# Optimization experiments

Measured on AMD Instinct MI355X. Metric: run time of the kernel, lower is better.

The kernel has to match this reference:

```python
import jax, jax.numpy as jnp
import numpy as np

B, L, H = 8, 4096, 1024
S = 32            # sentences (sep tokens) per sample, fixed for stackability
SEP_ID = 102      # BERT [SEP]
NUM_LABELS = 2
LN_EPS = 1e-5


def _make_ids_and_mask():
    rng = np.random.default_rng(0)
    ids = rng.integers(1000, 30000, size=(B, L))
    for i in range(B):
        pos = np.sort(rng.choice(np.arange(1, L), size=S, replace=False))
        ids[i, pos] = SEP_ID
    mask = np.ones((B, L), dtype=np.int32)
    return jnp.asarray(ids, dtype=jnp.int64), jnp.asarray(mask)


def setup_inputs() -> dict:
    key = jax.random.key(0)
    ks = jax.random.split(key, 4)
    input_ids, attention_mask = _make_ids_and_mask()
    std = 0.02
    return {
        "seq": jax.random.normal(ks[0], (B, L, H), dtype=jnp.float32),
        "input_ids": input_ids,
        "attention_mask": attention_mask,
        "W1": jax.random.normal(ks[1], (H, H), dtype=jnp.float32) * std,
        "b1": jnp.zeros((H,), jnp.float32),
        "ln_g": jnp.ones((H,), jnp.float32),
        "ln_b": jnp.zeros((H,), jnp.float32),
        "W2": jax.random.normal(ks[2], (H, NUM_LABELS), dtype=jnp.float32) * std,
        "b2": jnp.zeros((NUM_LABELS,), jnp.float32),
    }


def _segment_means(seq, input_ids, attention_mask):
    # sep positions per sample, fixed count S -> [B, S]
    sep_pos = jax.vmap(
        lambda ids: jnp.nonzero(ids == SEP_ID, size=S, fill_value=L - 1)[0]
    )(input_ids)
    bounds = jnp.concatenate(
        [jnp.zeros((seq.shape[0], 1), sep_pos.dtype), sep_pos], axis=1
    )  # [B, S+1]
    st, ed = bounds[:, :-1], bounds[:, 1:]  # inclusive span [st, ed]

    m = attention_mask.astype(seq.dtype)[..., None]            # [B,L,1]
    # exclusive prefix sums -> sum over [st, ed] = P[ed+1] - P[st]
    P = jnp.pad(jnp.cumsum(seq * m, axis=1), ((0, 0), (1, 0), (0, 0)))   # [B,L+1,H]
    C = jnp.pad(jnp.cumsum(attention_mask.astype(jnp.int32), axis=1), ((0, 0), (1, 0)))

    sums = (jnp.take_along_axis(P, (ed + 1)[..., None], axis=1)
            - jnp.take_along_axis(P, st[..., None], axis=1))   # [B,S,H]
    cnts = (jnp.take_along_axis(C, ed + 1, axis=1)
            - jnp.take_along_axis(C, st, axis=1))              # [B,S]
    cnts = jnp.maximum(cnts, 1).astype(seq.dtype)
    return sums / cnts[..., None]


def reference(seq, input_ids, attention_mask, W1, b1, ln_g, ln_b, W2, b2):
    reps = _segment_means(seq, input_ids, attention_mask)      # [B,S,H]
    h = jnp.einsum("bsh,hk->bsk", reps, W1) + b1
    mu = jnp.mean(h, axis=-1, keepdims=True)
    var = jnp.var(h, axis=-1, keepdims=True)
    h = (h - mu) * jax.lax.rsqrt(var + LN_EPS) * ln_g + ln_b
    h = jax.nn.gelu(h, approximate=False)   # torch nn.GELU default (erf); dropout is eval-mode identity
    return jnp.einsum("bsk,kn->bsn", h, W2) + b2               # [B,S,num_labels]
```

## Files before the change

### kernel.cpp

```cpp
#include <hip/hip_runtime.h>
#include <math.h>

#define BB 8
#define LL 4096
#define HH 1024
#define SS 32
#define SEPID 102
#define NROWS 256
#define TOK 64
#define SPLITK 8
#define KSLICE (HH / SPLITK)

__global__ __launch_bounds__(256) void prep_kernel(
    const int* __restrict__ ids, const int* __restrict__ mask,
    float* __restrict__ cnts, int* __restrict__ spos_g,
    float* __restrict__ sums) {
  int b = blockIdx.x;
  int by = blockIdx.y;
  int tid = threadIdx.x;
  if (by > 0) {
    int z = b * 8 + (by - 1);
    float4 zero = make_float4(0.f, 0.f, 0.f, 0.f);
    float4* p = (float4*)sums + (size_t)z * 1024;
#pragma unroll
    for (int i = 0; i < 4; i++) p[tid + i * 256] = zero;
    return;
  }
  __shared__ int spos_raw[SS];
  __shared__ int spos[SS];
  __shared__ int nsep;
  __shared__ int excl_s[257];
  __shared__ int wtot[4];
  if (tid == 0) nsep = 0;
  if (tid < SS) spos_raw[tid] = LL - 1;
  __syncthreads();
  const int* idb = ids + (size_t)b * LL;
  const int* mb  = mask + (size_t)b * LL;

  for (int t = tid; t < LL; t += 256) {
    if (idb[t] == SEPID) {
      int slot = atomicAdd(&nsep, 1);
      if (slot < SS) spos_raw[slot] = t;
    }
  }
  __syncthreads();
  if (tid < SS) {
    int p = spos_raw[tid];
    int rank = 0;
    for (int j = 0; j < SS; j++) {
      int q = spos_raw[j];
      rank += (q < p) || (q == p && j < tid);
    }
    spos[rank] = p;
  }

  int local = 0;
  int base = tid * 16;
#pragma unroll
  for (int i = 0; i < 16; i++) local += mb[base + i];
  int lane = tid & 63, wave = tid >> 6;
  int v = local;
#pragma unroll
  for (int off = 1; off < 64; off <<= 1) {
    int n = __shfl_up(v, off, 64);
    if (lane >= off) v += n;
  }
  if (lane == 63) wtot[wave] = v;
  __syncthreads();
  int woff = 0;
  for (int w = 0; w < wave; w++) woff += wtot[w];
  excl_s[tid] = woff + v - local;
  if (tid == 0) excl_s[256] = wtot[0] + wtot[1] + wtot[2] + wtot[3];
  __syncthreads();

  if (tid < SS) {
    spos_g[b * SS + tid] = spos[tid];
    int st = (tid == 0) ? 0 : spos[tid - 1];
    int ed = spos[tid];
    int pa = st, pb = ed + 1;
    int ca = excl_s[pa >> 4];
    for (int i = pa & ~15; i < pa; i++) ca += mb[i];
    int cb = excl_s[pb >> 4];
    for (int i = pb & ~15; i < pb; i++) cb += mb[i];
    cnts[b * SS + tid] = (float)max(cb - ca, 1);
  }
}

__device__ __forceinline__ void flush_seg(float* __restrict__ sums, int b,
                                          int seg, int tid, const float4& acc) {
  if (seg >= 0) {
    float* p = sums + ((size_t)(b * SS + seg)) * HH + tid * 4;
    atomicAdd(p + 0, acc.x);
    atomicAdd(p + 1, acc.y);
    atomicAdd(p + 2, acc.z);
    atomicAdd(p + 3, acc.w);
  }
}

__global__ __launch_bounds__(256) void segsum_kernel(
    const float4* __restrict__ seq, const int* __restrict__ mask,
    const int* __restrict__ spos_g, float* __restrict__ sums) {
  const int chunks = LL / TOK;
  int b = blockIdx.x / chunks;
  int c = blockIdx.x % chunks;
  int t0 = c * TOK;
  int tid = threadIdx.x;
  __shared__ int sposs[SS];
  __shared__ int scode[TOK];
  if (tid < SS) sposs[tid] = spos_g[b * SS + tid];
  __syncthreads();
  if (t0 > sposs[SS - 1]) return;
  if (tid < TOK) {
    int t = t0 + tid;
    int lo = 0, hi = SS;
    while (lo < hi) {
      int mid = (lo + hi) >> 1;
      if (sposs[mid] < t) lo = mid + 1; else hi = mid;
    }
    int issep = (lo < SS && sposs[lo] == t) ? 1 : 0;
    int r = lo;
    int m = mask[(size_t)b * LL + t];
    int live = (issep || r < SS) ? 1 : 0;
    scode[tid] = ((r << 1) | issep) | ((m && live) ? 0x100 : 0);
  }
  __syncthreads();
  float4 acc = make_float4(0.f, 0.f, 0.f, 0.f);
  int curseg = -1;
  const int rs = HH / 4;
  const float4* rowbase = seq + (size_t)(b * LL + t0) * rs + tid;
  float4 cur[4], nxt[4];
#pragma unroll
  for (int j = 0; j < 4; j++) cur[j] = rowbase[(size_t)j * rs];
  for (int g = 0; g < TOK / 4; g++) {
    int tb = g * 4;
    if (g < TOK / 4 - 1) {
#pragma unroll
      for (int j = 0; j < 4; j++) nxt[j] = rowbase[(size_t)(tb + 4 + j) * rs];
    }
#pragma unroll
    for (int j = 0; j < 4; j++) {
      int cd = scode[tb + j];
      int r = (cd >> 1) & 0x3F;
      int issep = cd & 1;
      float mf = (cd & 0x100) ? 1.f : 0.f;
      float4 v = cur[j];
      v.x *= mf; v.y *= mf; v.z *= mf; v.w *= mf;
      if (issep) {
        if (curseg != r) {
          flush_seg(sums, b, curseg, tid, acc);
          acc = make_float4(0.f, 0.f, 0.f, 0.f);
        }
        acc.x += v.x; acc.y += v.y; acc.z += v.z; acc.w += v.w;
        flush_seg(sums, b, r, tid, acc);
        if (r + 1 < SS) { curseg = r + 1; acc = v; }
        else { curseg = -1; acc = make_float4(0.f, 0.f, 0.f, 0.f); }
      } else {
        int sg = (r < SS) ? r : -1;
        if (sg != curseg) {
          flush_seg(sums, b, curseg, tid, acc);
          curseg = sg;
          acc = make_float4(0.f, 0.f, 0.f, 0.f);
        }
        acc.x += v.x; acc.y += v.y; acc.z += v.z; acc.w += v.w;
      }
    }
#pragma unroll
    for (int j = 0; j < 4; j++) cur[j] = nxt[j];
  }
  flush_seg(sums, b, curseg, tid, acc);
}

__global__ __launch_bounds__(256) void gemm1_kernel(
    const float* __restrict__ sums, const float* __restrict__ W1,
    float* __restrict__ h1p) {
  __shared__ float As[32][68];
  __shared__ float Bs[32][68];
  int bj = blockIdx.x;
  int bi = blockIdx.y;
  int bz = blockIdx.z;
  int tid = threadIdx.x;
  int r0 = bi * 64, c0 = bj * 64, kb = bz * KSLICE;

  int ai = tid >> 3;
  int af = tid & 7;
  int bk = tid >> 4;
  int bj4 = tid & 15;
  int tx = tid & 15, ty = tid >> 4;

  float acc[4][4];
#pragma unroll
  for (int i = 0; i < 4; i++)
#pragma unroll
    for (int j = 0; j < 4; j++) acc[i][j] = 0.f;

  for (int k0 = kb; k0 < kb + KSLICE; k0 += 32) {
    if (k0 != kb) __syncthreads();
    float4 a0 = *(const float4*)&sums[(size_t)(r0 + ai) * HH + k0 + af * 4];
    float4 a1 = *(const float4*)&sums[(size_t)(r0 + ai + 32) * HH + k0 + af * 4];
    float4 b0 = *(const float4*)&W1[(size_t)(k0 + bk) * HH + c0 + bj4 * 4];
    float4 b1 = *(const float4*)&W1[(size_t)(k0 + bk + 16) * HH + c0 + bj4 * 4];
    As[af * 4 + 0][ai] = a0.x;
    As[af * 4 + 1][ai] = a0.y;
    As[af * 4 + 2][ai] = a0.z;
    As[af * 4 + 3][ai] = a0.w;
    As[af * 4 + 0][ai + 32] = a1.x;
    As[af * 4 + 1][ai + 32] = a1.y;
    As[af * 4 + 2][ai + 32] = a1.z;
    As[af * 4 + 3][ai + 32] = a1.w;
    *(float4*)&Bs[bk][bj4 * 4] = b0;
    *(float4*)&Bs[bk + 16][bj4 * 4] = b1;
    __syncthreads();
#pragma unroll
    for (int kk = 0; kk < 32; kk++) {
      float4 a = *(const float4*)&As[kk][ty * 4];
      float4 b = *(const float4*)&Bs[kk][tx * 4];
      acc[0][0] += a.x * b.x; acc[0][1] += a.x * b.y;
      acc[0][2] += a.x * b.z; acc[0][3] += a.x * b.w;
      acc[1][0] += a.y * b.x; acc[1][1] += a.y * b.y;
      acc[1][2] += a.y * b.z; acc[1][3] += a.y * b.w;
      acc[2][0] += a.z * b.x; acc[2][1] += a.z * b.y;
      acc[2][2] += a.z * b.z; acc[2][3] += a.z * b.w;
      acc[3][0] += a.w * b.x; acc[3][1] += a.w * b.y;
      acc[3][2] += a.w * b.z; acc[3][3] += a.w * b.w;
    }
  }
#pragma unroll
  for (int dr = 0; dr < 4; dr++) {
    float4 o = make_float4(acc[dr][0], acc[dr][1], acc[dr][2], acc[dr][3]);
    *(float4*)&h1p[((size_t)bz * NROWS + r0 + ty * 4 + dr) * HH + c0 + tx * 4] = o;
  }
}

__global__ __launch_bounds__(256) void final_kernel(
    const float* __restrict__ h1p, const float* __restrict__ cnts,
    const float* __restrict__ b1, const float* __restrict__ ln_g,
    const float* __restrict__ ln_b, const float* __restrict__ W2,
    const float* __restrict__ b2, float* __restrict__ out) {
  int r = blockIdx.x;
  int tid = threadIdx.x;
  float4 x = make_float4(0.f, 0.f, 0.f, 0.f);
#pragma unroll
  for (int sl = 0; sl < SPLITK; sl++) {
    float4 p = ((const float4*)(h1p + ((size_t)sl * NROWS + r) * HH))[tid];
    x.x += p.x; x.y += p.y; x.z += p.z; x.w += p.w;
  }
  float invr = 1.0f / cnts[r];
  float4 bb1 = ((const float4*)b1)[tid];
  x.x = x.x * invr + bb1.x;
  x.y = x.y * invr + bb1.y;
  x.z = x.z * invr + bb1.z;
  x.w = x.w * invr + bb1.w;
  float s = x.x + x.y + x.z + x.w;
  float sq = x.x * x.x + x.y * x.y + x.z * x.z + x.w * x.w;
  __shared__ float redA[4], redB[4];
#pragma unroll
  for (int off = 32; off >= 1; off >>= 1) {
    s += __shfl_down(s, off, 64);
    sq += __shfl_down(sq, off, 64);
  }
  int wave = tid >> 6, lane = tid & 63;
  if (lane == 0) { redA[wave] = s; redB[wave] = sq; }
  __syncthreads();
  float ts = redA[0] + redA[1] + redA[2] + redA[3];
  float tq = redB[0] + redB[1] + redB[2] + redB[3];
  float mean = ts * (1.0f / HH);
  float var = tq * (1.0f / HH) - mean * mean;
  float rinv = rsqrtf(var + 1e-5f);
  float4 g4 = ((const float4*)ln_g)[tid];
  float4 bb4 = ((const float4*)ln_b)[tid];
  float4 w20 = ((const float4*)W2)[tid * 2];
  float4 w21 = ((const float4*)W2)[tid * 2 + 1];
  float xs[4] = {x.x, x.y, x.z, x.w};
  float gs[4] = {g4.x, g4.y, g4.z, g4.w};
  float bs[4] = {bb4.x, bb4.y, bb4.z, bb4.w};
  float w0[4] = {w20.x, w20.z, w21.x, w21.z};
  float w1[4] = {w20.y, w20.w, w21.y, w21.w};
  float o0 = 0.f, o1 = 0.f;
#pragma unroll
  for (int j = 0; j < 4; j++) {
    float y = (xs[j] - mean) * rinv * gs[j] + bs[j];
    float gel = 0.5f * y * (1.0f + erff(y * 0.70710678118654752440f));
    o0 += gel * w0[j];
    o1 += gel * w1[j];
  }
#pragma unroll
  for (int off = 32; off >= 1; off >>= 1) {
    o0 += __shfl_down(o0, off, 64);
    o1 += __shfl_down(o1, off, 64);
  }
  __syncthreads();
  if (lane == 0) { redA[wave] = o0; redB[wave] = o1; }
  __syncthreads();
  if (tid == 0) {
    out[(size_t)r * 2 + 0] = redA[0] + redA[1] + redA[2] + redA[3] + b2[0];
    out[(size_t)r * 2 + 1] = redB[0] + redB[1] + redB[2] + redB[3] + b2[1];
  }
}

extern "C" void kernel_launch(void* const* d_in, const int* in_sizes, int n_in,
                              void* d_out, int out_size, void* d_ws, size_t ws_size,
                              hipStream_t stream) {
  (void)in_sizes; (void)n_in; (void)out_size; (void)ws_size;
  const float* seq  = (const float*)d_in[0];
  const int*   ids  = (const int*)d_in[1];
  const int*   mask = (const int*)d_in[2];
  const float* W1   = (const float*)d_in[3];
  const float* b1   = (const float*)d_in[4];
  const float* ln_g = (const float*)d_in[5];
  const float* ln_b = (const float*)d_in[6];
  const float* W2   = (const float*)d_in[7];
  const float* b2   = (const float*)d_in[8];
  float* out = (float*)d_out;

  char* ws = (char*)d_ws;
  float* sums = (float*)ws;
  float* h1p  = (float*)(ws + (1 << 20));
  float* cnts = (float*)(ws + (9 << 20));
  int*   spos = (int*)(ws + (9 << 20) + 4096);

  dim3 gp(BB, 9);
  prep_kernel<<<gp, 256, 0, stream>>>(ids, mask, cnts, spos, sums);
  segsum_kernel<<<BB * (LL / TOK), 256, 0, stream>>>(
      (const float4*)seq, mask, spos, sums);
  dim3 g1(16, 4, SPLITK);
  gemm1_kernel<<<g1, 256, 0, stream>>>(sums, W1, h1p);
  final_kernel<<<NROWS, 256, 0, stream>>>(h1p, cnts, b1, ln_g, ln_b, W2, b2, out);
}
```

Measured before the change: 235.0 us.

## Vectorize prep scans, halve segsum chunk, add fast path, prefetch gemm1 tiles

The prep kernel now reads ids and mask as int4 vectors. The segment-sum kernel drops to 32 tokens per block, gets an occupancy hint in its launch bounds, and gains a fast path that sums four rows at once when they share one unmasked non-separator segment. gemm1 now loads the next K tile into registers before computing on the current shared-memory tile, a software pipelining step. Together these aim to cut memory latency and branch overhead in the bandwidth-bound segment sum. Smaller chunks add more blocks and more atomic flushes, and the launch-bounds hint may constrain register allocation.

```diff
diff --git a/kernel.cpp b/kernel.cpp
--- a/kernel.cpp
+++ b/kernel.cpp
@@ -7,7 +7,7 @@
 #define SS 32
 #define SEPID 102
 #define NROWS 256
-#define TOK 64
+#define TOK 32
 #define SPLITK 8
 #define KSLICE (HH / SPLITK)
 
@@ -37,11 +37,15 @@
   const int* idb = ids + (size_t)b * LL;
   const int* mb  = mask + (size_t)b * LL;
 
-  for (int t = tid; t < LL; t += 256) {
-    if (idb[t] == SEPID) {
-      int slot = atomicAdd(&nsep, 1);
-      if (slot < SS) spos_raw[slot] = t;
-    }
+  const int4* id4 = (const int4*)idb;
+#pragma unroll
+  for (int it = 0; it < 4; it++) {
+    int t4 = tid + it * 256;
+    int4 w = id4[t4];
+    if (w.x == SEPID) { int s = atomicAdd(&nsep, 1); if (s < SS) spos_raw[s] = t4 * 4 + 0; }
+    if (w.y == SEPID) { int s = atomicAdd(&nsep, 1); if (s < SS) spos_raw[s] = t4 * 4 + 1; }
+    if (w.z == SEPID) { int s = atomicAdd(&nsep, 1); if (s < SS) spos_raw[s] = t4 * 4 + 2; }
+    if (w.w == SEPID) { int s = atomicAdd(&nsep, 1); if (s < SS) spos_raw[s] = t4 * 4 + 3; }
   }
   __syncthreads();
   if (tid < SS) {
@@ -54,10 +58,13 @@
     spos[rank] = p;
   }
 
+  const int4* m4 = (const int4*)mb;
   int local = 0;
-  int base = tid * 16;
-#pragma unroll
-  for (int i = 0; i < 16; i++) local += mb[base + i];
+#pragma unroll
+  for (int i = 0; i < 4; i++) {
+    int4 w = m4[tid * 4 + i];
+    local += w.x + w.y + w.z + w.w;
+  }
   int lane = tid & 63, wave = tid >> 6;
   int v = local;
 #pragma unroll
@@ -97,7 +104,7 @@
   }
 }
 
-__global__ __launch_bounds__(256) void segsum_kernel(
+__global__ __launch_bounds__(256, 4) void segsum_kernel(
     const float4* __restrict__ seq, const int* __restrict__ mask,
     const int* __restrict__ spos_g, float* __restrict__ sums) {
   const int chunks = LL / TOK;
@@ -137,31 +144,50 @@
 #pragma unroll
       for (int j = 0; j < 4; j++) nxt[j] = rowbase[(size_t)(tb + 4 + j) * rs];
     }
-#pragma unroll
-    for (int j = 0; j < 4; j++) {
-      int cd = scode[tb + j];
-      int r = (cd >> 1) & 0x3F;
-      int issep = cd & 1;
-      float mf = (cd & 0x100) ? 1.f : 0.f;
-      float4 v = cur[j];
-      v.x *= mf; v.y *= mf; v.z *= mf; v.w *= mf;
-      if (issep) {
-        if (curseg != r) {
-          flush_seg(sums, b, curseg, tid, acc);
-          acc = make_float4(0.f, 0.f, 0.f, 0.f);
+    int4 cd4 = *(const int4*)&scode[tb];
+    bool fast = (cd4.x == cd4.y) & (cd4.x == cd4.z) & (cd4.x == cd4.w) &
+                ((cd4.x & 1) == 0) & ((cd4.x & 0x100) != 0);
+    if (fast) {
+      int r = (cd4.x >> 1) & 0x3F;
+      if (r != curseg) {
+        flush_seg(sums, b, curseg, tid, acc);
+        curseg = r;
+        acc = make_float4(0.f, 0.f, 0.f, 0.f);
+      }
+      float4 s01, s23;
+      s01.x = cur[0].x + cur[1].x; s01.y = cur[0].y + cur[1].y;
+      s01.z = cur[0].z + cur[1].z; s01.w = cur[0].w + cur[1].w;
+      s23.x = cur[2].x + cur[3].x; s23.y = cur[2].y + cur[3].y;
+      s23.z = cur[2].z + cur[3].z; s23.w = cur[2].w + cur[3].w;
+      acc.x += s01.x + s23.x; acc.y += s01.y + s23.y;
+      acc.z += s01.z + s23.z; acc.w += s01.w + s23.w;
+    } else {
+#pragma unroll
+      for (int j = 0; j < 4; j++) {
+        int cd = scode[tb + j];
+        int r = (cd >> 1) & 0x3F;
+        int issep = cd & 1;
+        float mf = (cd & 0x100) ? 1.f : 0.f;
+        float4 v = cur[j];
+        v.x *= mf; v.y *= mf; v.z *= mf; v.w *= mf;
+        if (issep) {
+          if (curseg != r) {
+            flush_seg(sums, b, curseg, tid, acc);
+            acc = make_float4(0.f, 0.f, 0.f, 0.f);
+          }
+          acc.x += v.x; acc.y += v.y; acc.z += v.z; acc.w += v.w;
+          flush_seg(sums, b, r, tid, acc);
+          if (r + 1 < SS) { curseg = r + 1; acc = v; }
+          else { curseg = -1; acc = make_float4(0.f, 0.f, 0.f, 0.f); }
+        } else {
+          int sg = (r < SS) ? r : -1;
+          if (sg != curseg) {
+            flush_seg(sums, b, curseg, tid, acc);
+            curseg = sg;
+            acc = make_float4(0.f, 0.f, 0.f, 0.f);
+          }
+          acc.x += v.x; acc.y += v.y; acc.z += v.z; acc.w += v.w;
         }
-        acc.x += v.x; acc.y += v.y; acc.z += v.z; acc.w += v.w;
-        flush_seg(sums, b, r, tid, acc);
-        if (r + 1 < SS) { curseg = r + 1; acc = v; }
-        else { curseg = -1; acc = make_float4(0.f, 0.f, 0.f, 0.f); }
-      } else {
-        int sg = (r < SS) ? r : -1;
-        if (sg != curseg) {
-          flush_seg(sums, b, curseg, tid, acc);
-          curseg = sg;
-          acc = make_float4(0.f, 0.f, 0.f, 0.f);
-        }
-        acc.x += v.x; acc.y += v.y; acc.z += v.z; acc.w += v.w;
       }
     }
 #pragma unroll
@@ -193,12 +219,19 @@
 #pragma unroll
     for (int j = 0; j < 4; j++) acc[i][j] = 0.f;
 
-  for (int k0 = kb; k0 < kb + KSLICE; k0 += 32) {
-    if (k0 != kb) __syncthreads();
-    float4 a0 = *(const float4*)&sums[(size_t)(r0 + ai) * HH + k0 + af * 4];
-    float4 a1 = *(const float4*)&sums[(size_t)(r0 + ai + 32) * HH + k0 + af * 4];
-    float4 b0 = *(const float4*)&W1[(size_t)(k0 + bk) * HH + c0 + bj4 * 4];
-    float4 b1 = *(const float4*)&W1[(size_t)(k0 + bk + 16) * HH + c0 + bj4 * 4];
+  const float* aptr0 = &sums[(size_t)(r0 + ai) * HH + af * 4];
+  const float* aptr1 = aptr0 + (size_t)32 * HH;
+  const float* bptr0 = &W1[(size_t)bk * HH + c0 + bj4 * 4];
+  const float* bptr1 = bptr0 + (size_t)16 * HH;
+
+  float4 a0 = *(const float4*)(aptr0 + kb);
+  float4 a1 = *(const float4*)(aptr1 + kb);
+  float4 b0 = *(const float4*)(bptr0 + (size_t)kb * HH);
+  float4 b1 = *(const float4*)(bptr1 + (size_t)kb * HH);
+
+#pragma unroll
+  for (int ks = 0; ks < KSLICE / 32; ks++) {
+    if (ks) __syncthreads();
     As[af * 4 + 0][ai] = a0.x;
     As[af * 4 + 1][ai] = a0.y;
     As[af * 4 + 2][ai] = a0.z;
@@ -209,6 +242,11 @@
     As[af * 4 + 3][ai + 32] = a1.w;
     *(float4*)&Bs[bk][bj4 * 4] = b0;
     *(float4*)&Bs[bk + 16][bj4 * 4] = b1;
+    int kn = kb + (ks + 1 < KSLICE / 32 ? (ks + 1) * 32 : ks * 32);
+    float4 na0 = *(const float4*)(aptr0 + kn);
+    float4 na1 = *(const float4*)(aptr1 + kn);
+    float4 nb0 = *(const float4*)(bptr0 + (size_t)kn * HH);
+    float4 nb1 = *(const float4*)(bptr1 + (size_t)kn * HH);
     __syncthreads();
 #pragma unroll
     for (int kk = 0; kk < 32; kk++) {
@@ -223,6 +261,7 @@
       acc[3][0] += a.w * b.x; acc[3][1] += a.w * b.y;
       acc[3][2] += a.w * b.z; acc[3][3] += a.w * b.w;
     }
+    a0 = na0; a1 = na1; b0 = nb0; b1 = nb1;
   }
 #pragma unroll
   for (int dr = 0; dr < 4; dr++) {
```

Result: faster. 230.3 us (-2.0%).
